# Kernel optimization log

Measured on AMD Instinct MI355X. Metric: run time of the kernel, lower is better.

The kernel has to match this reference:

```python
import jax, jax.numpy as jnp
import numpy as np

B, L, DM, H = 1, 2048, 3072, 24
D = DM // H            # 128 head dim
MLP = 4 * DM           # 12288
EPS = 1e-6


def setup_inputs() -> dict:
    key = jax.random.key(0)
    ks = jax.random.split(key, 12)
    s = lambda fan_in: 1.0 / np.sqrt(fan_in)
    return {
        "x": jax.random.normal(ks[0], (B, L, DM), jnp.float32),
        "vec": jax.random.normal(ks[1], (B, DM), jnp.float32),
        "pe": jax.random.normal(ks[2], (1, 1, L, D // 2, 2, 2), jnp.float32),
        # Modulation linear: dim -> 3*dim
        "mod_w": jax.random.normal(ks[3], (DM, 3 * DM), jnp.float32) * s(DM),
        "mod_b": jnp.zeros((3 * DM,), jnp.float32),
        # linear1: dim -> 3*dim + mlp
        "lin1_w": jax.random.normal(ks[4], (DM, 3 * DM + MLP), jnp.float32) * s(DM),
        "lin1_b": jnp.zeros((3 * DM + MLP,), jnp.float32),
        # linear2: dim + mlp -> dim
        "lin2_w": jax.random.normal(ks[5], (DM + MLP, DM), jnp.float32) * s(DM + MLP),
        "lin2_b": jnp.zeros((DM,), jnp.float32),
        # QKNorm RMS scales (per head_dim)
        "q_scale": jnp.ones((D,), jnp.float32),
        "k_scale": jnp.ones((D,), jnp.float32),
    }


def _rms_norm(t, scale):
    # RMSNorm over last dim (head_dim), eps 1e-6
    rrms = jax.lax.rsqrt(jnp.mean(jnp.square(t), axis=-1, keepdims=True) + EPS)
    return t * rrms * scale


def _apply_rope(t, pe):
    # t: (B,H,L,D); pe: (1,1,L,D/2,2,2) as in flux apply_rope
    t2 = t.reshape(B, H, L, D // 2, 1, 2)
    out = pe[..., 0] * t2[..., 0] + pe[..., 1] * t2[..., 1]  # (B,H,L,D/2,2)
    return out.reshape(B, H, L, D)


def reference(x, vec, pe, mod_w, mod_b, lin1_w, lin1_b, lin2_w, lin2_b, q_scale, k_scale):
    # Modulation: Linear(silu(vec)) -> shift, scale, gate, each (B,1,DM)
    mod = jax.nn.silu(vec) @ mod_w + mod_b
    shift, scale, gate = jnp.split(mod[:, None, :], 3, axis=-1)

    # pre_norm: LayerNorm without affine, eps 1e-6
    mu = jnp.mean(x, axis=-1, keepdims=True)
    var = jnp.mean(jnp.square(x - mu), axis=-1, keepdims=True)
    xn = (x - mu) * jax.lax.rsqrt(var + EPS)
    x_mod = (1.0 + scale) * xn + shift

    # fused QKV + MLP projection
    h = x_mod @ lin1_w + lin1_b
    qkv, mlp = h[..., : 3 * DM], h[..., 3 * DM :]
    qkv = qkv.reshape(B, L, 3, H, D).transpose(2, 0, 3, 1, 4)  # (3,B,H,L,D)
    q, k, v = qkv[0], qkv[1], qkv[2]

    q = _rms_norm(q, q_scale)
    k = _rms_norm(k, k_scale)
    q = _apply_rope(q, pe)
    k = _apply_rope(k, pe)

    # scaled dot-product attention (non-causal, SDPA default scale)
    scores = jnp.einsum("bhqd,bhkd->bhqk", q, k) * (1.0 / np.sqrt(D))
    attn = jax.nn.softmax(scores, axis=-1)
    o = jnp.einsum("bhqk,bhkd->bhqd", attn, v)
    o = o.transpose(0, 2, 1, 3).reshape(B, L, DM)  # B H L D -> B L (H D)

    out = jnp.concatenate([o, jax.nn.gelu(mlp, approximate=True)], axis=-1) @ lin2_w + lin2_b
    return x + gate * out
```

## Files before the change

### kernel.cpp

```cpp
#include <hip/hip_runtime.h>
#include <math.h>

#define LQ 2048
#define DMODEL 3072
#define NHEADS 24
#define DHEADC 128
#define NQKV 9216
#define NOUT1 21504
#define KIN2 15360
#define EPSV 1e-6f

typedef __attribute__((ext_vector_type(8))) short short8;
typedef __attribute__((ext_vector_type(4))) short short4v;
typedef __attribute__((ext_vector_type(4))) float f32x4;

__device__ __forceinline__ short f2bf(float f) {
  unsigned int u = __float_as_uint(f);
  unsigned int r = (u + 0x7fffu + ((u >> 16) & 1u)) >> 16;
  return (short)(unsigned short)r;
}

__device__ __forceinline__ float geluf(float v) {
  float inner = 0.7978845608028654f * (v + 0.044715f * v * v * v);
  return 0.5f * v * (1.0f + tanhf(inner));
}

__device__ __forceinline__ void async_ld16(void* lds, const void* g) {
  __builtin_amdgcn_global_load_lds(
      (const __attribute__((address_space(1))) unsigned int*)g,
      (__attribute__((address_space(3))) unsigned int*)lds, 16, 0, 0);
}

__global__ __launch_bounds__(256) void k_wconv(const float* __restrict__ w,
                                               short* __restrict__ wt,
                                               int K, int N) {
  __shared__ float tile[32][33];
  int bk = blockIdx.x * 32, bn = blockIdx.y * 32;
  int t = threadIdx.x;
  int r = t >> 3, c = (t & 7) * 4;
  float4 v = *reinterpret_cast<const float4*>(w + (size_t)(bk + r) * N + bn + c);
  tile[r][c + 0] = v.x; tile[r][c + 1] = v.y; tile[r][c + 2] = v.z; tile[r][c + 3] = v.w;
  __syncthreads();
  short4v o;
  o[0] = f2bf(tile[c + 0][r]); o[1] = f2bf(tile[c + 1][r]);
  o[2] = f2bf(tile[c + 2][r]); o[3] = f2bf(tile[c + 3][r]);
  *reinterpret_cast<short4v*>(wt + (size_t)(bn + r) * K + bk + c) = o;
}

__global__ __launch_bounds__(256) void k_modpart(const float* __restrict__ vec,
                                                 const float* __restrict__ mod_w,
                                                 float* __restrict__ partial) {
  __shared__ float sv[128];
  int t = threadIdx.x;
  int nb = blockIdx.x * 256;
  int kb = blockIdx.y * 128;
  if (t < 128) { float z = vec[kb + t]; sv[t] = z / (1.0f + expf(-z)); }
  __syncthreads();
  const float* wp = mod_w + (size_t)kb * NQKV + nb + t;
  float acc = 0.0f;
#pragma unroll 8
  for (int k = 0; k < 128; k++) acc += sv[k] * wp[(size_t)k * NQKV];
  partial[(size_t)blockIdx.y * NQKV + nb + t] = acc;
}

__global__ __launch_bounds__(256) void k_modred(const float* __restrict__ partial,
                                                const float* __restrict__ mod_b,
                                                float* __restrict__ modv) {
  int n = blockIdx.x * 256 + threadIdx.x;
  float acc = mod_b[n];
#pragma unroll
  for (int ky = 0; ky < 24; ky++) acc += partial[(size_t)ky * NQKV + n];
  modv[n] = acc;
}

__global__ __launch_bounds__(256) void k_ln(const float* __restrict__ x,
                                            const float* __restrict__ modv,
                                            short* __restrict__ xmod) {
  int l = blockIdx.x, t = threadIdx.x;
  const float* xr = x + (size_t)l * DMODEL;
  const float4* xr4 = (const float4*)xr;
  float4 vbuf[3];
  float s = 0.f, ss = 0.f;
#pragma unroll
  for (int i = 0; i < 3; i++) {
    float4 v = xr4[t + i * 256];
    vbuf[i] = v;
    s += v.x + v.y + v.z + v.w;
    ss += v.x * v.x + v.y * v.y + v.z * v.z + v.w * v.w;
  }
#pragma unroll
  for (int m = 32; m >= 1; m >>= 1) { s += __shfl_xor(s, m); ss += __shfl_xor(ss, m); }
  __shared__ float red[8];
  __shared__ float stats[2];
  int wave = t >> 6;
  if ((t & 63) == 0) { red[wave] = s; red[4 + wave] = ss; }
  __syncthreads();
  if (t == 0) {
    float st = red[0] + red[1] + red[2] + red[3];
    float sst = red[4] + red[5] + red[6] + red[7];
    float mu = st / DMODEL;
    float var = sst / DMODEL - mu * mu;
    stats[0] = mu; stats[1] = rsqrtf(var + EPSV);
  }
  __syncthreads();
  float mu = stats[0], rr = stats[1];
#pragma unroll
  for (int i = 0; i < 3; i++) {
    float4 v = vbuf[i];
    int c = (t + i * 256) * 4;
    short4v o;
    o[0] = f2bf((1.f + modv[DMODEL + c + 0]) * ((v.x - mu) * rr) + modv[c + 0]);
    o[1] = f2bf((1.f + modv[DMODEL + c + 1]) * ((v.y - mu) * rr) + modv[c + 1]);
    o[2] = f2bf((1.f + modv[DMODEL + c + 2]) * ((v.z - mu) * rr) + modv[c + 2]);
    o[3] = f2bf((1.f + modv[DMODEL + c + 3]) * ((v.w - mu) * rr) + modv[c + 3]);
    *(short4v*)(xmod + (size_t)l * DMODEL + c) = o;
  }
}

#define G1_NT 48
#define G1_NITER 24
#define G2_KC 3840
#define G2_NT 60
#define G2_NITER 30

__device__ __forceinline__ void ldA4(short8 af[4][2], const short* ldsA, int rbase,
                                     int lrow, const int* kOff) {
#pragma unroll
  for (int m = 0; m < 4; m++)
#pragma unroll
    for (int ks = 0; ks < 2; ks++)
      af[m][ks] = *(const short8*)&ldsA[(rbase + m * 16 + lrow) * 64 + kOff[ks]];
}

__device__ __forceinline__ void ldB2(short8 bfr[2][2], const short* ldsB, int rbase,
                                     int lrow, const int* kOff) {
#pragma unroll
  for (int n = 0; n < 2; n++)
#pragma unroll
    for (int ks = 0; ks < 2; ks++)
      bfr[n][ks] = *(const short8*)&ldsB[(rbase + n * 16 + lrow) * 64 + kOff[ks]];
}

__device__ __forceinline__ void stage_halfA(short* ldsT, const short* G, int rowbase,
                                            int tauB, int half, int wid, int srow, int sk,
                                            size_t strideB) {
#pragma unroll
  for (int c = 0; c < 2; c++) {
    int j = c * 8 + wid;
    int row0 = ((j >> 3) << 7) + half * 64 + ((j & 7) << 3);
    const char* src = (const char*)G +
                      (size_t)(rowbase + row0 + srow) * strideB + tauB + sk;
    async_ld16(ldsT + row0 * 64, src);
  }
}

__device__ __forceinline__ void stage_halfB(short* ldsT, const short* G, int rowbase,
                                            int tauB, int half, int wid, int srow, int sk,
                                            size_t strideB) {
#pragma unroll
  for (int c = 0; c < 2; c++) {
    int j = c * 8 + wid;
    int row0 = ((j >> 2) << 6) + half * 32 + ((j & 3) << 3);
    const char* src = (const char*)G +
                      (size_t)(rowbase + row0 + srow) * strideB + tauB + sk;
    async_ld16(ldsT + row0 * 64, src);
  }
}

#define SYNC_MFMA(mh, nh, VM)                                                       \
  do {                                                                              \
    if (VM) asm volatile("s_waitcnt vmcnt(6)" ::: "memory");                        \
    __builtin_amdgcn_s_barrier();                                                   \
    asm volatile("s_waitcnt lgkmcnt(0)" ::: "memory");                              \
    __builtin_amdgcn_sched_barrier(0);                                              \
    __builtin_amdgcn_s_setprio(1);                                                  \
    _Pragma("unroll") for (int m_ = 0; m_ < 4; m_++)                                \
      _Pragma("unroll") for (int n_ = 0; n_ < 2; n_++)                              \
        _Pragma("unroll") for (int k_ = 0; k_ < 2; k_++)                            \
          acc[(mh) * 4 + m_][(nh) * 2 + n_] =                                       \
              __builtin_amdgcn_mfma_f32_16x16x32_bf16(                              \
                  af[m_][k_], bfr[n_][k_], acc[(mh) * 4 + m_][(nh) * 2 + n_], 0, 0, 0); \
    __builtin_amdgcn_s_setprio(0);                                                  \
    __builtin_amdgcn_s_barrier();                                                   \
  } while (0)

#define G1_TB(tt) ((((tt) < G1_NT) ? (tt) : (G1_NT - 1)) * 128)
#define G2_TB(tt) ((((tt) < G2_NT) ? (tt) : (G2_NT - 1)) * 128)

__global__ __launch_bounds__(512, 2) void k_gemm1_8p(const short* __restrict__ A,
                                                     const short* __restrict__ Bt,
                                                     const float* __restrict__ bias,
                                                     float* __restrict__ qraw,
                                                     float* __restrict__ kraw,
                                                     short* __restrict__ vt,
                                                     short* __restrict__ a2) {
  __shared__ __align__(16) short lds[2][2][256 * 64];
  int t = threadIdx.x;
  int wid = t >> 6, lane = t & 63;
  int bid = blockIdx.x;
  int swzb = (bid & 7) * 84 + (bid >> 3);
  int bm = (swzb & 7) << 8;
  int bn = (swzb >> 3) << 8;
  int wm_ = (wid >> 2) << 7;
  int wn_ = (wid & 3) << 6;
  int lrow = lane & 15;
  int swzx = (lane & 7) << 4;
  int kOff[2];
#pragma unroll
  for (int ks = 0; ks < 2; ks++) kOff[ks] = ((ks * 64 + (lane >> 4) * 16) ^ swzx) >> 1;
  int srow = lane >> 3;
  int sk = ((lane & 7) * 16) ^ (srow << 4);
  const size_t strA = (size_t)(DMODEL * 2);

  short* A0p = &lds[0][0][0];
  short* B0p = &lds[0][1][0];
  short* A1p = &lds[1][0][0];
  short* B1p = &lds[1][1][0];

  f32x4 zero = {0.f, 0.f, 0.f, 0.f};
  f32x4 acc[8][4];
#pragma unroll
  for (int i = 0; i < 8; i++)
#pragma unroll
    for (int j = 0; j < 4; j++) acc[i][j] = zero;
  short8 af[4][2], bfr[2][2];

  stage_halfA(A0p, A, bm, 0, 0, wid, srow, sk, strA);
  stage_halfA(A0p, A, bm, 0, 1, wid, srow, sk, strA);
  stage_halfB(B0p, Bt, bn, 0, 0, wid, srow, sk, strA);
  stage_halfB(B0p, Bt, bn, 0, 1, wid, srow, sk, strA);
  stage_halfA(A1p, A, bm, 128, 0, wid, srow, sk, strA);
  stage_halfB(B1p, Bt, bn, 128, 1, wid, srow, sk, strA);
  stage_halfA(A1p, A, bm, 128, 1, wid, srow, sk, strA);
  asm volatile("s_waitcnt vmcnt(6)" ::: "memory");
  __builtin_amdgcn_s_barrier();

#pragma unroll 1
  for (int it = 0; it < G1_NITER; ++it) {
    int T = it * 2;
    ldA4(af, A0p, wm_, lrow, kOff);
    ldB2(bfr, B0p, wn_, lrow, kOff);
    stage_halfB(B1p, Bt, bn, G1_TB(T + 1), 0, wid, srow, sk, strA);
    SYNC_MFMA(0, 0, 0);
    ldB2(bfr, B0p, wn_ + 32, lrow, kOff);
    stage_halfA(A0p, A, bm, G1_TB(T + 2), 0, wid, srow, sk, strA);
    SYNC_MFMA(0, 1, 0);
    ldA4(af, A0p, wm_ + 64, lrow, kOff);
    stage_halfB(B0p, Bt, bn, G1_TB(T + 2), 1, wid, srow, sk, strA);
    SYNC_MFMA(1, 1, 0);
    ldB2(bfr, B0p, wn_, lrow, kOff);
    stage_halfA(A0p, A, bm, G1_TB(T + 2), 1, wid, srow, sk, strA);
    SYNC_MFMA(1, 0, 1);
    ldA4(af, A1p, wm_, lrow, kOff);
    ldB2(bfr, B1p, wn_, lrow, kOff);
    stage_halfB(B0p, Bt, bn, G1_TB(T + 2), 0, wid, srow, sk, strA);
    SYNC_MFMA(0, 0, 0);
    ldB2(bfr, B1p, wn_ + 32, lrow, kOff);
    stage_halfA(A1p, A, bm, G1_TB(T + 3), 0, wid, srow, sk, strA);
    SYNC_MFMA(0, 1, 0);
    ldA4(af, A1p, wm_ + 64, lrow, kOff);
    stage_halfB(B1p, Bt, bn, G1_TB(T + 3), 1, wid, srow, sk, strA);
    SYNC_MFMA(1, 1, 0);
    ldB2(bfr, B1p, wn_, lrow, kOff);
    stage_halfA(A1p, A, bm, G1_TB(T + 3), 1, wid, srow, sk, strA);
    SYNC_MFMA(1, 0, 1);
  }

  int r0 = bm + wm_ + ((lane >> 4) << 2);
  int c0 = bn + wn_ + lrow;
#pragma unroll
  for (int an = 0; an < 4; an++) {
    int col = c0 + an * 16;
    float bb = bias[col];
#pragma unroll
    for (int am = 0; am < 8; am++) {
#pragma unroll
      for (int r = 0; r < 4; r++) {
        float v = acc[am][an][r] + bb;
        int row = r0 + am * 16 + r;
        if (col < NQKV) {
          int s = col / DMODEL;
          int rem = col - s * DMODEL;
          int hh = rem >> 7, d = rem & 127;
          if (s == 0)      qraw[((size_t)hh * LQ + row) * DHEADC + d] = v;
          else if (s == 1) kraw[((size_t)hh * LQ + row) * DHEADC + d] = v;
          else             vt[((size_t)hh * DHEADC + d) * LQ + row] = f2bf(v);
        } else {
          a2[(size_t)row * KIN2 + DMODEL + (col - NQKV)] = f2bf(geluf(v));
        }
      }
    }
  }
}

__global__ __launch_bounds__(512, 2) void k_gemm2_8p(const short* __restrict__ A,
                                                     const short* __restrict__ Bt,
                                                     float* __restrict__ part) {
  __shared__ __align__(16) short lds[2][2][256 * 64];
  int t = threadIdx.x;
  int wid = t >> 6, lane = t & 63;
  int bid = blockIdx.x;
  int swzb = (bid & 7) * 48 + (bid >> 3);
  int bmIdx = swzb & 7;
  int g = swzb >> 3;
  int bnIdx = g % 12;
  int s = g / 12;
  int bm = bmIdx << 8;
  int bn = bnIdx << 8;
  const short* Ab = A + (size_t)s * G2_KC;
  const short* Bb = Bt + (size_t)s * G2_KC;
  float* Pb = part + (size_t)s * LQ * DMODEL;
  int wm_ = (wid >> 2) << 7;
  int wn_ = (wid & 3) << 6;
  int lrow = lane & 15;
  int swzx = (lane & 7) << 4;
  int kOff[2];
#pragma unroll
  for (int ks = 0; ks < 2; ks++) kOff[ks] = ((ks * 64 + (lane >> 4) * 16) ^ swzx) >> 1;
  int srow = lane >> 3;
  int sk = ((lane & 7) * 16) ^ (srow << 4);
  const size_t strA = (size_t)(KIN2 * 2);

  short* A0p = &lds[0][0][0];
  short* B0p = &lds[0][1][0];
  short* A1p = &lds[1][0][0];
  short* B1p = &lds[1][1][0];

  f32x4 zero = {0.f, 0.f, 0.f, 0.f};
  f32x4 acc[8][4];
#pragma unroll
  for (int i = 0; i < 8; i++)
#pragma unroll
    for (int j = 0; j < 4; j++) acc[i][j] = zero;
  short8 af[4][2], bfr[2][2];

  stage_halfA(A0p, Ab, bm, 0, 0, wid, srow, sk, strA);
  stage_halfA(A0p, Ab, bm, 0, 1, wid, srow, sk, strA);
  stage_halfB(B0p, Bb, bn, 0, 0, wid, srow, sk, strA);
  stage_halfB(B0p, Bb, bn, 0, 1, wid, srow, sk, strA);
  stage_halfA(A1p, Ab, bm, 128, 0, wid, srow, sk, strA);
  stage_halfB(B1p, Bb, bn, 128, 1, wid, srow, sk, strA);
  stage_halfA(A1p, Ab, bm, 128, 1, wid, srow, sk, strA);
  asm volatile("s_waitcnt vmcnt(6)" ::: "memory");
  __builtin_amdgcn_s_barrier();

#pragma unroll 1
  for (int it = 0; it < G2_NITER; ++it) {
    int T = it * 2;
    ldA4(af, A0p, wm_, lrow, kOff);
    ldB2(bfr, B0p, wn_, lrow, kOff);
    stage_halfB(B1p, Bb, bn, G2_TB(T + 1), 0, wid, srow, sk, strA);
    SYNC_MFMA(0, 0, 0);
    ldB2(bfr, B0p, wn_ + 32, lrow, kOff);
    stage_halfA(A0p, Ab, bm, G2_TB(T + 2), 0, wid, srow, sk, strA);
    SYNC_MFMA(0, 1, 0);
    ldA4(af, A0p, wm_ + 64, lrow, kOff);
    stage_halfB(B0p, Bb, bn, G2_TB(T + 2), 1, wid, srow, sk, strA);
    SYNC_MFMA(1, 1, 0);
    ldB2(bfr, B0p, wn_, lrow, kOff);
    stage_halfA(A0p, Ab, bm, G2_TB(T + 2), 1, wid, srow, sk, strA);
    SYNC_MFMA(1, 0, 1);
    ldA4(af, A1p, wm_, lrow, kOff);
    ldB2(bfr, B1p, wn_, lrow, kOff);
    stage_halfB(B0p, Bb, bn, G2_TB(T + 2), 0, wid, srow, sk, strA);
    SYNC_MFMA(0, 0, 0);
    ldB2(bfr, B1p, wn_ + 32, lrow, kOff);
    stage_halfA(A1p, Ab, bm, G2_TB(T + 3), 0, wid, srow, sk, strA);
    SYNC_MFMA(0, 1, 0);
    ldA4(af, A1p, wm_ + 64, lrow, kOff);
    stage_halfB(B1p, Bb, bn, G2_TB(T + 3), 1, wid, srow, sk, strA);
    SYNC_MFMA(1, 1, 0);
    ldB2(bfr, B1p, wn_, lrow, kOff);
    stage_halfA(A1p, Ab, bm, G2_TB(T + 3), 1, wid, srow, sk, strA);
    SYNC_MFMA(1, 0, 1);
  }

  int r0 = bm + wm_ + ((lane >> 4) << 2);
  int c0 = bn + wn_ + lrow;
#pragma unroll
  for (int an = 0; an < 4; an++) {
    int col = c0 + an * 16;
#pragma unroll
    for (int am = 0; am < 8; am++) {
#pragma unroll
      for (int r = 0; r < 4; r++) {
        int row = r0 + am * 16 + r;
        Pb[(size_t)row * DMODEL + col] = acc[am][an][r];
      }
    }
  }
}

__global__ __launch_bounds__(256) void k_g2red(const float* __restrict__ part,
                                               const float* __restrict__ bias,
                                               const float* __restrict__ x,
                                               const float* __restrict__ gate,
                                               float* __restrict__ out) {
  int idx = blockIdx.x * 256 + threadIdx.x;
  int c4 = idx % (DMODEL / 4);
  const float4* p4 = (const float4*)part;
  const size_t st4 = (size_t)LQ * DMODEL / 4;
  float4 s0 = p4[idx];
  float4 s1 = p4[idx + st4];
  float4 s2 = p4[idx + 2 * st4];
  float4 s3 = p4[idx + 3 * st4];
  float4 b4 = ((const float4*)bias)[c4];
  float4 g4 = ((const float4*)gate)[c4];
  float4 x4 = ((const float4*)x)[idx];
  float4 o;
  o.x = x4.x + g4.x * (b4.x + s0.x + s1.x + s2.x + s3.x);
  o.y = x4.y + g4.y * (b4.y + s0.y + s1.y + s2.y + s3.y);
  o.z = x4.z + g4.z * (b4.z + s0.z + s1.z + s2.z + s3.z);
  o.w = x4.w + g4.w * (b4.w + s0.w + s1.w + s2.w + s3.w);
  ((float4*)out)[idx] = o;
}

__global__ __launch_bounds__(256) void k_qkprep(const float* __restrict__ qraw,
                                                const float* __restrict__ kraw,
                                                const float* __restrict__ pe,
                                                const float* __restrict__ q_scale,
                                                const float* __restrict__ k_scale,
                                                short* __restrict__ qn,
                                                short* __restrict__ kn) {
  int wave = threadIdx.x >> 6, lane = threadIdx.x & 63;
  int l = blockIdx.x * 4 + wave;
  int h = blockIdx.y;
  int isK = blockIdx.z;
  const float* src = (isK ? kraw : qraw) + ((size_t)h * LQ + l) * DHEADC;
  const float* sc  = isK ? k_scale : q_scale;
  short* dst = (isK ? kn : qn) + ((size_t)h * LQ + l) * DHEADC;
  float2 tv = *(const float2*)(src + lane * 2);
  float ssq = tv.x * tv.x + tv.y * tv.y;
#pragma unroll
  for (int m = 1; m < 64; m <<= 1) ssq += __shfl_xor(ssq, m);
  float rr = rsqrtf(ssq * (1.0f / 128.0f) + EPSV);
  float t0 = tv.x * rr * sc[lane * 2];
  float t1 = tv.y * rr * sc[lane * 2 + 1];
  float4 p4 = *(const float4*)(pe + ((size_t)l * 64 + lane) * 4);
  float o0 = p4.x * t0 + p4.y * t1;
  float o1 = p4.z * t0 + p4.w * t1;
  if (!isK) { o0 *= 0.08838834764831845f; o1 *= 0.08838834764831845f; }
  dst[lane * 2] = f2bf(o0);
  dst[lane * 2 + 1] = f2bf(o1);
}

__global__ __launch_bounds__(256) void k_flash(const short* __restrict__ qn,
                                               const short* __restrict__ kn,
                                               const short* __restrict__ vt,
                                               short* __restrict__ a2) {
  __shared__ short Qs[128][136];
  __shared__ short Ks[32][136];
  __shared__ short Vs[128][40];
  __shared__ short Ps[4][32][40];
  int t = threadIdx.x;
  int qb = blockIdx.x * 128, h = blockIdx.y;
  int wave = t >> 6, lane = t & 63;
  int lrow = lane & 15, lko = (lane >> 4) * 8;
  int wm = wave * 32;
  const short* qbase = qn + ((size_t)h * LQ + qb) * DHEADC;
#pragma unroll
  for (int i = 0; i < 8; i++) {
    int idx = i * 256 + t;
    int row = idx >> 4, c = (idx & 15) * 8;
    *(short8*)&Qs[row][c] = *(const short8*)(qbase + (size_t)row * DHEADC + c);
  }
  f32x4 zero = {0.f, 0.f, 0.f, 0.f};
  f32x4 oacc[2][8];
#pragma unroll
  for (int i = 0; i < 2; i++)
#pragma unroll
    for (int j = 0; j < 8; j++) oacc[i][j] = zero;
  float mI[2][4], lI[2][4];
#pragma unroll
  for (int i = 0; i < 2; i++)
#pragma unroll
    for (int r = 0; r < 4; r++) { mI[i][r] = -1e30f; lI[i][r] = 0.f; }
  __syncthreads();
  for (int kt = 0; kt < 64; kt++) {
    int krow0 = kt * 32;
#pragma unroll
    for (int i = 0; i < 2; i++) {
      int idx = i * 256 + t;
      int row = idx >> 4, c = (idx & 15) * 8;
      *(short8*)&Ks[row][c] = *(const short8*)(kn + ((size_t)h * LQ + krow0 + row) * DHEADC + c);
    }
#pragma unroll
    for (int i = 0; i < 2; i++) {
      int idx = i * 256 + t;
      int d = idx >> 2, c = (idx & 3) * 8;
      *(short8*)&Vs[d][c] = *(const short8*)(vt + ((size_t)h * DHEADC + d) * LQ + krow0 + c);
    }
    __syncthreads();
    f32x4 sacc[2][2];
#pragma unroll
    for (int i = 0; i < 2; i++)
#pragma unroll
      for (int j = 0; j < 2; j++) sacc[i][j] = zero;
#pragma unroll
    for (int kk = 0; kk < 4; kk++) {
      short8 qa[2], kb[2];
#pragma unroll
      for (int i = 0; i < 2; i++) qa[i] = *(const short8*)&Qs[wm + i * 16 + lrow][kk * 32 + lko];
#pragma unroll
      for (int j = 0; j < 2; j++) kb[j] = *(const short8*)&Ks[j * 16 + lrow][kk * 32 + lko];
#pragma unroll
      for (int i = 0; i < 2; i++)
#pragma unroll
        for (int j = 0; j < 2; j++)
          sacc[i][j] = __builtin_amdgcn_mfma_f32_16x16x32_bf16(qa[i], kb[j], sacc[i][j], 0, 0, 0);
    }
#pragma unroll
    for (int i = 0; i < 2; i++) {
      float al[4];
#pragma unroll
      for (int r = 0; r < 4; r++) {
        float mx = fmaxf(sacc[i][0][r], sacc[i][1][r]);
#pragma unroll
        for (int m = 1; m < 16; m <<= 1) mx = fmaxf(mx, __shfl_xor(mx, m));
        float mnew = fmaxf(mI[i][r], mx);
        float alpha = exp2f((mI[i][r] - mnew) * 1.4426950408889634f);
        float p0 = exp2f((sacc[i][0][r] - mnew) * 1.4426950408889634f);
        float p1 = exp2f((sacc[i][1][r] - mnew) * 1.4426950408889634f);
        sacc[i][0][r] = p0; sacc[i][1][r] = p1;
        float rs = p0 + p1;
#pragma unroll
        for (int m = 1; m < 16; m <<= 1) rs += __shfl_xor(rs, m);
        lI[i][r] = lI[i][r] * alpha + rs;
        mI[i][r] = mnew;
        al[r] = alpha;
      }
#pragma unroll
      for (int j = 0; j < 8; j++) {
        f32x4 o = oacc[i][j];
        o[0] *= al[0]; o[1] *= al[1]; o[2] *= al[2]; o[3] *= al[3];
        oacc[i][j] = o;
      }
#pragma unroll
      for (int j = 0; j < 2; j++)
#pragma unroll
        for (int r = 0; r < 4; r++)
          Ps[wave][i * 16 + (lane >> 4) * 4 + r][j * 16 + lrow] = f2bf(sacc[i][j][r]);
    }
    short8 pa[2];
#pragma unroll
    for (int i = 0; i < 2; i++) pa[i] = *(const short8*)&Ps[wave][i * 16 + lrow][lko];
#pragma unroll
    for (int j = 0; j < 8; j++) {
      short8 vb = *(const short8*)&Vs[j * 16 + lrow][lko];
#pragma unroll
      for (int i = 0; i < 2; i++)
        oacc[i][j] = __builtin_amdgcn_mfma_f32_16x16x32_bf16(pa[i], vb, oacc[i][j], 0, 0, 0);
    }
    __syncthreads();
  }
#pragma unroll
  for (int i = 0; i < 2; i++) {
    float inv[4];
#pragma unroll
    for (int r = 0; r < 4; r++) inv[r] = 1.0f / lI[i][r];
#pragma unroll
    for (int j = 0; j < 8; j++) {
#pragma unroll
      for (int r = 0; r < 4; r++) {
        int row = qb + wm + i * 16 + (lane >> 4) * 4 + r;
        int col = h * DHEADC + j * 16 + lrow;
        a2[(size_t)row * KIN2 + col] = f2bf(oacc[i][j][r] * inv[r]);
      }
    }
  }
}

extern "C" void kernel_launch(void* const* d_in, const int* in_sizes, int n_in,
                              void* d_out, int out_size, void* d_ws, size_t ws_size,
                              hipStream_t stream) {
  (void)in_sizes; (void)n_in; (void)out_size; (void)ws_size;
  const float* x       = (const float*)d_in[0];
  const float* vec     = (const float*)d_in[1];
  const float* pe      = (const float*)d_in[2];
  const float* mod_w   = (const float*)d_in[3];
  const float* mod_b   = (const float*)d_in[4];
  const float* lin1_w  = (const float*)d_in[5];
  const float* lin1_b  = (const float*)d_in[6];
  const float* lin2_w  = (const float*)d_in[7];
  const float* lin2_b  = (const float*)d_in[8];
  const float* q_scale = (const float*)d_in[9];
  const float* k_scale = (const float*)d_in[10];
  float* out = (float*)d_out;

  char* base = (char*)d_ws;
  size_t off = 0;
  auto carve = [&](size_t bytes) -> void* {
    void* q = base + off;
    off += (bytes + 255) & ~(size_t)255;
    return q;
  };
  short* W1t  = (short*)carve((size_t)NOUT1 * DMODEL * 2);
  short* xmod = (short*)carve((size_t)LQ * DMODEL * 2);
  float* qraw = (float*)carve((size_t)NHEADS * LQ * DHEADC * 4);
  float* kraw = (float*)carve((size_t)NHEADS * LQ * DHEADC * 4);
  short* qnb  = (short*)carve((size_t)NHEADS * LQ * DHEADC * 2);
  short* knb  = (short*)carve((size_t)NHEADS * LQ * DHEADC * 2);
  short* vtb  = (short*)carve((size_t)NHEADS * LQ * DHEADC * 2);
  short* a2   = (short*)carve((size_t)LQ * KIN2 * 2);
  float* modv = (float*)carve((size_t)NQKV * 4);
  float* part = (float*)carve((size_t)24 * NQKV * 4);
  float* g2part = (float*)xmod;

  k_wconv<<<dim3(DMODEL / 32, NOUT1 / 32), 256, 0, stream>>>(lin1_w, W1t, DMODEL, NOUT1);
  k_modpart<<<dim3(NQKV / 256, 24), 256, 0, stream>>>(vec, mod_w, part);
  k_modred<<<NQKV / 256, 256, 0, stream>>>(part, mod_b, modv);
  k_ln<<<LQ, 256, 0, stream>>>(x, modv, xmod);
  k_gemm1_8p<<<dim3((LQ / 256) * (NOUT1 / 256)), 512, 0, stream>>>(xmod, W1t, lin1_b,
                                                                   qraw, kraw, vtb, a2);
  k_wconv<<<dim3(KIN2 / 32, DMODEL / 32), 256, 0, stream>>>(lin2_w, W1t, KIN2, DMODEL);
  k_qkprep<<<dim3(LQ / 4, NHEADS, 2), 256, 0, stream>>>(qraw, kraw, pe, q_scale, k_scale, qnb, knb);
  k_flash<<<dim3(LQ / 128, NHEADS), 256, 0, stream>>>(qnb, knb, vtb, a2);
  k_gemm2_8p<<<dim3(384), 512, 0, stream>>>(a2, W1t, g2part);
  k_g2red<<<dim3((LQ * DMODEL / 4) / 256), 256, 0, stream>>>(g2part, lin2_b, x,
                                                             modv + 2 * DMODEL, out);
}
```

Before: 1.476 ms.

## Double-buffer B fragments in GEMM mainloops and raise GEMM2 split-K to five

The GEMM mainloops now use two B-fragment register sets, so B fragments are reused across the M-halves instead of being reloaded from LDS. A partial lgkmcnt wait is added so LDS reads can overlap the barrier. GEMM2 split-K goes from 4 to 5 slices (480 blocks instead of 384), which gives the 256 CUs better occupancy. The fifth partial goes to spare workspace after the converted weights, and the reduction kernel now reads five partials, adding extra memory traffic.

```diff
diff --git a/kernel.cpp b/kernel.cpp
--- a/kernel.cpp
+++ b/kernel.cpp
@@ -119,9 +119,10 @@
 
 #define G1_NT 48
 #define G1_NITER 24
-#define G2_KC 3840
-#define G2_NT 60
-#define G2_NITER 30
+#define G2_S 5
+#define G2_KC 3072
+#define G2_NT 48
+#define G2_NITER 24
 
 __device__ __forceinline__ void ldA4(short8 af[4][2], const short* ldsA, int rbase,
                                      int lrow, const int* kOff) {
@@ -167,9 +168,10 @@
   }
 }
 
-#define SYNC_MFMA(mh, nh, VM)                                                       \
+#define SYNC_MFMA(mh, nh, B, VM, LH)                                                \
   do {                                                                              \
     if (VM) asm volatile("s_waitcnt vmcnt(6)" ::: "memory");                        \
+    if (LH) asm volatile("s_waitcnt lgkmcnt(8)" ::: "memory");                      \
     __builtin_amdgcn_s_barrier();                                                   \
     asm volatile("s_waitcnt lgkmcnt(0)" ::: "memory");                              \
     __builtin_amdgcn_sched_barrier(0);                                              \
@@ -179,7 +181,7 @@
         _Pragma("unroll") for (int k_ = 0; k_ < 2; k_++)                            \
           acc[(mh) * 4 + m_][(nh) * 2 + n_] =                                       \
               __builtin_amdgcn_mfma_f32_16x16x32_bf16(                              \
-                  af[m_][k_], bfr[n_][k_], acc[(mh) * 4 + m_][(nh) * 2 + n_], 0, 0, 0); \
+                  af[m_][k_], (B)[n_][k_], acc[(mh) * 4 + m_][(nh) * 2 + n_], 0, 0, 0); \
     __builtin_amdgcn_s_setprio(0);                                                  \
     __builtin_amdgcn_s_barrier();                                                   \
   } while (0)
@@ -223,7 +225,7 @@
   for (int i = 0; i < 8; i++)
 #pragma unroll
     for (int j = 0; j < 4; j++) acc[i][j] = zero;
-  short8 af[4][2], bfr[2][2];
+  short8 af[4][2], bf0[2][2], bf1[2][2];
 
   stage_halfA(A0p, A, bm, 0, 0, wid, srow, sk, strA);
   stage_halfA(A0p, A, bm, 0, 1, wid, srow, sk, strA);
@@ -239,31 +241,29 @@
   for (int it = 0; it < G1_NITER; ++it) {
     int T = it * 2;
     ldA4(af, A0p, wm_, lrow, kOff);
-    ldB2(bfr, B0p, wn_, lrow, kOff);
+    ldB2(bf0, B0p, wn_, lrow, kOff);
     stage_halfB(B1p, Bt, bn, G1_TB(T + 1), 0, wid, srow, sk, strA);
-    SYNC_MFMA(0, 0, 0);
-    ldB2(bfr, B0p, wn_ + 32, lrow, kOff);
+    SYNC_MFMA(0, 0, bf0, 0, 1);
+    ldB2(bf1, B0p, wn_ + 32, lrow, kOff);
     stage_halfA(A0p, A, bm, G1_TB(T + 2), 0, wid, srow, sk, strA);
-    SYNC_MFMA(0, 1, 0);
+    SYNC_MFMA(0, 1, bf1, 0, 0);
     ldA4(af, A0p, wm_ + 64, lrow, kOff);
     stage_halfB(B0p, Bt, bn, G1_TB(T + 2), 1, wid, srow, sk, strA);
-    SYNC_MFMA(1, 1, 0);
-    ldB2(bfr, B0p, wn_, lrow, kOff);
+    SYNC_MFMA(1, 1, bf1, 0, 0);
     stage_halfA(A0p, A, bm, G1_TB(T + 2), 1, wid, srow, sk, strA);
-    SYNC_MFMA(1, 0, 1);
+    SYNC_MFMA(1, 0, bf0, 1, 0);
     ldA4(af, A1p, wm_, lrow, kOff);
-    ldB2(bfr, B1p, wn_, lrow, kOff);
+    ldB2(bf0, B1p, wn_, lrow, kOff);
     stage_halfB(B0p, Bt, bn, G1_TB(T + 2), 0, wid, srow, sk, strA);
-    SYNC_MFMA(0, 0, 0);
-    ldB2(bfr, B1p, wn_ + 32, lrow, kOff);
+    SYNC_MFMA(0, 0, bf0, 0, 1);
+    ldB2(bf1, B1p, wn_ + 32, lrow, kOff);
     stage_halfA(A1p, A, bm, G1_TB(T + 3), 0, wid, srow, sk, strA);
-    SYNC_MFMA(0, 1, 0);
+    SYNC_MFMA(0, 1, bf1, 0, 0);
     ldA4(af, A1p, wm_ + 64, lrow, kOff);
     stage_halfB(B1p, Bt, bn, G1_TB(T + 3), 1, wid, srow, sk, strA);
-    SYNC_MFMA(1, 1, 0);
-    ldB2(bfr, B1p, wn_, lrow, kOff);
+    SYNC_MFMA(1, 1, bf1, 0, 0);
     stage_halfA(A1p, A, bm, G1_TB(T + 3), 1, wid, srow, sk, strA);
-    SYNC_MFMA(1, 0, 1);
+    SYNC_MFMA(1, 0, bf0, 1, 0);
   }
 
   int r0 = bm + wm_ + ((lane >> 4) << 2);
@@ -295,12 +295,13 @@
 
 __global__ __launch_bounds__(512, 2) void k_gemm2_8p(const short* __restrict__ A,
                                                      const short* __restrict__ Bt,
-                                                     float* __restrict__ part) {
+                                                     float* __restrict__ part,
+                                                     float* __restrict__ part4) {
   __shared__ __align__(16) short lds[2][2][256 * 64];
   int t = threadIdx.x;
   int wid = t >> 6, lane = t & 63;
   int bid = blockIdx.x;
-  int swzb = (bid & 7) * 48 + (bid >> 3);
+  int swzb = (bid & 7) * 60 + (bid >> 3);
   int bmIdx = swzb & 7;
   int g = swzb >> 3;
   int bnIdx = g % 12;
@@ -309,7 +310,7 @@
   int bn = bnIdx << 8;
   const short* Ab = A + (size_t)s * G2_KC;
   const short* Bb = Bt + (size_t)s * G2_KC;
-  float* Pb = part + (size_t)s * LQ * DMODEL;
+  float* Pb = (s < 4) ? part + (size_t)s * LQ * DMODEL : part4;
   int wm_ = (wid >> 2) << 7;
   int wn_ = (wid & 3) << 6;
   int lrow = lane & 15;
@@ -332,7 +333,7 @@
   for (int i = 0; i < 8; i++)
 #pragma unroll
     for (int j = 0; j < 4; j++) acc[i][j] = zero;
-  short8 af[4][2], bfr[2][2];
+  short8 af[4][2], bf0[2][2], bf1[2][2];
 
   stage_halfA(A0p, Ab, bm, 0, 0, wid, srow, sk, strA);
   stage_halfA(A0p, Ab, bm, 0, 1, wid, srow, sk, strA);
@@ -348,31 +349,29 @@
   for (int it = 0; it < G2_NITER; ++it) {
     int T = it * 2;
     ldA4(af, A0p, wm_, lrow, kOff);
-    ldB2(bfr, B0p, wn_, lrow, kOff);
+    ldB2(bf0, B0p, wn_, lrow, kOff);
     stage_halfB(B1p, Bb, bn, G2_TB(T + 1), 0, wid, srow, sk, strA);
-    SYNC_MFMA(0, 0, 0);
-    ldB2(bfr, B0p, wn_ + 32, lrow, kOff);
+    SYNC_MFMA(0, 0, bf0, 0, 1);
+    ldB2(bf1, B0p, wn_ + 32, lrow, kOff);
     stage_halfA(A0p, Ab, bm, G2_TB(T + 2), 0, wid, srow, sk, strA);
-    SYNC_MFMA(0, 1, 0);
+    SYNC_MFMA(0, 1, bf1, 0, 0);
     ldA4(af, A0p, wm_ + 64, lrow, kOff);
     stage_halfB(B0p, Bb, bn, G2_TB(T + 2), 1, wid, srow, sk, strA);
-    SYNC_MFMA(1, 1, 0);
-    ldB2(bfr, B0p, wn_, lrow, kOff);
+    SYNC_MFMA(1, 1, bf1, 0, 0);
     stage_halfA(A0p, Ab, bm, G2_TB(T + 2), 1, wid, srow, sk, strA);
-    SYNC_MFMA(1, 0, 1);
+    SYNC_MFMA(1, 0, bf0, 1, 0);
     ldA4(af, A1p, wm_, lrow, kOff);
-    ldB2(bfr, B1p, wn_, lrow, kOff);
+    ldB2(bf0, B1p, wn_, lrow, kOff);
     stage_halfB(B0p, Bb, bn, G2_TB(T + 2), 0, wid, srow, sk, strA);
-    SYNC_MFMA(0, 0, 0);
-    ldB2(bfr, B1p, wn_ + 32, lrow, kOff);
+    SYNC_MFMA(0, 0, bf0, 0, 1);
+    ldB2(bf1, B1p, wn_ + 32, lrow, kOff);
     stage_halfA(A1p, Ab, bm, G2_TB(T + 3), 0, wid, srow, sk, strA);
-    SYNC_MFMA(0, 1, 0);
+    SYNC_MFMA(0, 1, bf1, 0, 0);
     ldA4(af, A1p, wm_ + 64, lrow, kOff);
     stage_halfB(B1p, Bb, bn, G2_TB(T + 3), 1, wid, srow, sk, strA);
-    SYNC_MFMA(1, 1, 0);
-    ldB2(bfr, B1p, wn_, lrow, kOff);
+    SYNC_MFMA(1, 1, bf1, 0, 0);
     stage_halfA(A1p, Ab, bm, G2_TB(T + 3), 1, wid, srow, sk, strA);
-    SYNC_MFMA(1, 0, 1);
+    SYNC_MFMA(1, 0, bf0, 1, 0);
   }
 
   int r0 = bm + wm_ + ((lane >> 4) << 2);
@@ -392,6 +391,7 @@
 }
 
 __global__ __launch_bounds__(256) void k_g2red(const float* __restrict__ part,
+                                               const float* __restrict__ part4,
                                                const float* __restrict__ bias,
                                                const float* __restrict__ x,
                                                const float* __restrict__ gate,
@@ -404,14 +404,15 @@
   float4 s1 = p4[idx + st4];
   float4 s2 = p4[idx + 2 * st4];
   float4 s3 = p4[idx + 3 * st4];
+  float4 s4 = ((const float4*)part4)[idx];
   float4 b4 = ((const float4*)bias)[c4];
   float4 g4 = ((const float4*)gate)[c4];
   float4 x4 = ((const float4*)x)[idx];
   float4 o;
-  o.x = x4.x + g4.x * (b4.x + s0.x + s1.x + s2.x + s3.x);
-  o.y = x4.y + g4.y * (b4.y + s0.y + s1.y + s2.y + s3.y);
-  o.z = x4.z + g4.z * (b4.z + s0.z + s1.z + s2.z + s3.z);
-  o.w = x4.w + g4.w * (b4.w + s0.w + s1.w + s2.w + s3.w);
+  o.x = x4.x + g4.x * (b4.x + s0.x + s1.x + s2.x + s3.x + s4.x);
+  o.y = x4.y + g4.y * (b4.y + s0.y + s1.y + s2.y + s3.y + s4.y);
+  o.z = x4.z + g4.z * (b4.z + s0.z + s1.z + s2.z + s3.z + s4.z);
+  o.w = x4.w + g4.w * (b4.w + s0.w + s1.w + s2.w + s3.w + s4.w);
   ((float4*)out)[idx] = o;
 }
 
@@ -605,6 +606,7 @@
   float* modv = (float*)carve((size_t)NQKV * 4);
   float* part = (float*)carve((size_t)24 * NQKV * 4);
   float* g2part = (float*)xmod;
+  float* g2p4   = (float*)((char*)W1t + (size_t)DMODEL * KIN2 * 2);
 
   k_wconv<<<dim3(DMODEL / 32, NOUT1 / 32), 256, 0, stream>>>(lin1_w, W1t, DMODEL, NOUT1);
   k_modpart<<<dim3(NQKV / 256, 24), 256, 0, stream>>>(vec, mod_w, part);
@@ -615,7 +617,7 @@
   k_wconv<<<dim3(KIN2 / 32, DMODEL / 32), 256, 0, stream>>>(lin2_w, W1t, KIN2, DMODEL);
   k_qkprep<<<dim3(LQ / 4, NHEADS, 2), 256, 0, stream>>>(qraw, kraw, pe, q_scale, k_scale, qnb, knb);
   k_flash<<<dim3(LQ / 128, NHEADS), 256, 0, stream>>>(qnb, knb, vtb, a2);
-  k_gemm2_8p<<<dim3(384), 512, 0, stream>>>(a2, W1t, g2part);
-  k_g2red<<<dim3((LQ * DMODEL / 4) / 256), 256, 0, stream>>>(g2part, lin2_b, x,
+  k_gemm2_8p<<<dim3(96 * G2_S), 512, 0, stream>>>(a2, W1t, g2part, g2p4);
+  k_g2red<<<dim3((LQ * DMODEL / 4) / 256), 256, 0, stream>>>(g2part, g2p4, lin2_b, x,
                                                              modv + 2 * DMODEL, out);
 }
```

Result: slower. 1.907 ms (+29.2%).
